# Performance work log

Measured on AMD Instinct MI355X. Metric: run time of the kernel, lower is better.

## Reference

```python
import jax, jax.numpy as jnp
import numpy as np

DIM = 1024
INTER = 2048
N_EXPERTS = 8
TOP_K = 2
ROUTE_SCALE = 1.0


def setup_inputs() -> dict:
    key = jax.random.key(0)
    ks = jax.random.split(key, 4)
    x = jax.random.normal(ks[0], (4, 2048, DIM), dtype=jnp.float32)
    # Gate weight matches nn.Parameter(torch.randn(n_experts, dim))
    Wg = jax.random.normal(ks[1], (N_EXPERTS, DIM), dtype=jnp.float32)
    W1 = jax.random.normal(ks[2], (N_EXPERTS, DIM, INTER), dtype=jnp.float32) * (1.0 / np.sqrt(DIM))
    b1 = jnp.zeros((N_EXPERTS, INTER), dtype=jnp.float32)
    W2 = jax.random.normal(ks[3], (N_EXPERTS, INTER, DIM), dtype=jnp.float32) * (1.0 / np.sqrt(INTER))
    b2 = jnp.zeros((N_EXPERTS, DIM), dtype=jnp.float32)
    return {"x": x, "Wg": Wg, "W1": W1, "b1": b1, "W2": W2, "b2": b2}


def reference(x, Wg, W1, b1, W2, b2):
    # Flatten tokens: [T, D]
    xt = x.reshape(-1, DIM)
    T = xt.shape[0]

    # --- Gate: sigmoid scores, top-k, normalized weights ---
    scores = jax.nn.sigmoid(xt @ Wg.T)                       # [T, E]
    top_w, top_idx = jax.lax.top_k(scores, TOP_K)            # [T, K]
    top_w = top_w / jnp.sum(top_w, axis=-1, keepdims=True)
    top_w = top_w * ROUTE_SCALE

    # Sparse combine weights [T, E] (top_k indices are distinct per token)
    cw = jnp.zeros((T, N_EXPERTS), dtype=xt.dtype)
    cw = cw.at[jnp.arange(T)[:, None], top_idx].set(top_w)

    # --- Experts: dense per-expert MLP, weighted combine ---
    # (dropout is identity in eval mode)
    h = jax.nn.relu(jnp.einsum('td,edh->eth', xt, W1) + b1[:, None, :])   # [E, T, H]
    eo = jnp.einsum('eth,ehd->etd', h, W2) + b2[:, None, :]               # [E, T, D]
    y = jnp.einsum('etd,te->td', eo, cw)                                  # [T, D]
    return y
```

## Files before the change

### kernel.cpp

```cpp
#include <hip/hip_runtime.h>
#include <stdint.h>

#define DIM   1024
#define INTER 2048
#define NEXP  8
#define TIMAX 136

typedef _Float16 f16;
typedef __attribute__((ext_vector_type(2))) _Float16 f16x2;
typedef __attribute__((ext_vector_type(4))) _Float16 f16x4;
typedef __attribute__((ext_vector_type(8))) _Float16 f16x8;
typedef __attribute__((ext_vector_type(4))) float    f32x4;

static __device__ __forceinline__ void gload16(const void* gsrc, void* lds) {
    __builtin_amdgcn_global_load_lds(
        (const __attribute__((address_space(1))) uint32_t*)gsrc,
        (__attribute__((address_space(3))) uint32_t*)lds,
        16, 0, 0);
}

__device__ __forceinline__ void transpose_tile(const float* __restrict__ W, f16* __restrict__ Wt,
                                               int K, int N, int e, int kb, int nb, int t,
                                               f16 (*tile)[66]) {
    const float* We  = W  + (size_t)e * K * N;
    f16*         Wte = Wt + (size_t)e * K * N;
    const int kl = t >> 4;
    const int nq = t & 15;
    #pragma unroll
    for (int pass = 0; pass < 4; ++pass) {
        int k = pass * 16 + kl;
        float4 v = *(const float4*)&We[(size_t)(kb + k) * N + nb + nq * 4];
        f16x2 lo = { (f16)v.x, (f16)v.y };
        f16x2 hi = { (f16)v.z, (f16)v.w };
        *(f16x2*)&tile[k][nq * 4]     = lo;
        *(f16x2*)&tile[k][nq * 4 + 2] = hi;
    }
    __syncthreads();
    const int n  = t >> 2;
    const int kq = t & 3;
    f16x8 o0, o1;
    #pragma unroll
    for (int i = 0; i < 8; ++i) o0[i] = tile[kq * 16 + i][n];
    #pragma unroll
    for (int i = 0; i < 8; ++i) o1[i] = tile[kq * 16 + 8 + i][n];
    f16* dst = &Wte[(size_t)(nb + n) * K + kb + kq * 16];
    *(f16x8*)dst       = o0;
    *(f16x8*)(dst + 8) = o1;
}

__global__ void preprocess_kernel(const float* __restrict__ x, const float* __restrict__ Wg,
                                  const float* __restrict__ W1, const float* __restrict__ W2,
                                  f16* __restrict__ xh, f16* __restrict__ w1t, f16* __restrict__ w2t,
                                  float* __restrict__ gw, int* __restrict__ gidx, int T) {
    __shared__ f16 tile[64][66];
    const int bid     = blockIdx.x;
    const int NB_GATE = T / 4;
    const int NB_TR1  = (INTER / 64) * (DIM / 64) * NEXP;

    if (bid < NB_GATE) {
        const int tid  = threadIdx.x;
        const int tok  = bid * 4 + (tid >> 6);
        const int lane = tid & 63;
        const float4* xr  = (const float4*)(x + (size_t)tok * DIM);
        f16*          xhr = xh + (size_t)tok * DIM;
        float s[NEXP];
        #pragma unroll
        for (int e = 0; e < NEXP; ++e) s[e] = 0.f;
        #pragma unroll
        for (int it = 0; it < 4; ++it) {
            int i = it * 64 + lane;
            float4 xv = xr[i];
            f16x4 hv = { (f16)xv.x, (f16)xv.y, (f16)xv.z, (f16)xv.w };
            *(f16x4*)(xhr + i * 4) = hv;
            #pragma unroll
            for (int e = 0; e < NEXP; ++e) {
                float4 wv = ((const float4*)(Wg + e * DIM))[i];
                s[e] += xv.x * wv.x + xv.y * wv.y + xv.z * wv.z + xv.w * wv.w;
            }
        }
        #pragma unroll
        for (int e = 0; e < NEXP; ++e) {
            #pragma unroll
            for (int off = 32; off > 0; off >>= 1) s[e] += __shfl_xor(s[e], off);
        }
        if (lane == 0) {
            float sc[NEXP];
            #pragma unroll
            for (int e = 0; e < NEXP; ++e) sc[e] = 1.f / (1.f + expf(-s[e]));
            int i0 = 0;
            #pragma unroll
            for (int e = 1; e < NEXP; ++e) if (sc[e] > sc[i0]) i0 = e;
            int i1 = -1;
            #pragma unroll
            for (int e = 0; e < NEXP; ++e) if (e != i0 && (i1 < 0 || sc[e] > sc[i1])) i1 = e;
            float w0 = sc[i0], w1 = sc[i1];
            float inv = 1.f / (w0 + w1);
            gw[2 * tok + 0] = w0 * inv;
            gw[2 * tok + 1] = w1 * inv;
            gidx[2 * tok + 0] = i0;
            gidx[2 * tok + 1] = i1;
        }
    } else if (bid < NB_GATE + NB_TR1) {
        const int b  = bid - NB_GATE;
        const int nx = b % (INTER / 64);
        const int ky = (b / (INTER / 64)) % (DIM / 64);
        const int e  = b / ((INTER / 64) * (DIM / 64));
        transpose_tile(W1, w1t, DIM, INTER, e, ky * 64, nx * 64, threadIdx.x, tile);
    } else {
        const int b  = bid - NB_GATE - NB_TR1;
        const int nx = b % (DIM / 64);
        const int ky = (b / (DIM / 64)) % (INTER / 64);
        const int e  = b / ((DIM / 64) * (INTER / 64));
        transpose_tile(W2, w2t, INTER, DIM, e, ky * 64, nx * 64, threadIdx.x, tile);
    }
}

__global__ __launch_bounds__(1024)
void route_kernel(const int* __restrict__ gidx, int* __restrict__ offsets,
                  int* __restrict__ tor, int* __restrict__ ros,
                  int* __restrict__ tileE, int* __restrict__ tileR0, int T) {
    const int tid  = threadIdx.x;
    const int lane = tid & 63;
    const int wv   = tid >> 6;
    const int NE   = 2 * T;
    __shared__ int wc[16][NEXP];
    __shared__ int rb[NEXP];

    int c[NEXP];
    #pragma unroll
    for (int e = 0; e < NEXP; ++e) c[e] = 0;
    for (int i = tid; i < NE; i += 1024) {
        int g = gidx[i];
        #pragma unroll
        for (int e = 0; e < NEXP; ++e) c[e] += (g == e) ? 1 : 0;
    }
    #pragma unroll
    for (int e = 0; e < NEXP; ++e) {
        #pragma unroll
        for (int off = 32; off > 0; off >>= 1) c[e] += __shfl_xor(c[e], off);
    }
    if (lane == 0) {
        #pragma unroll
        for (int e = 0; e < NEXP; ++e) wc[wv][e] = c[e];
    }
    __syncthreads();
    if (tid == 0) {
        int acc = 0;
        for (int e = 0; e < NEXP; ++e) {
            int t = 0;
            for (int w2 = 0; w2 < 16; ++w2) t += wc[w2][e];
            offsets[e] = acc;
            rb[e] = acc;
            acc += t;
        }
        offsets[NEXP] = acc;
        int nt = 0;
        for (int e = 0; e < NEXP; ++e)
            for (int r0 = offsets[e]; r0 < offsets[e + 1]; r0 += 128) {
                tileE[nt]  = e;
                tileR0[nt] = r0;
                ++nt;
            }
        for (; nt < TIMAX; ++nt) { tileE[nt] = -1; tileR0[nt] = 0; }
    }
    __syncthreads();

    for (int base = 0; base < NE; base += 1024) {
        int i = base + tid;
        int g = gidx[i];
        int myrank = 0;
        #pragma unroll
        for (int e = 0; e < NEXP; ++e) {
            unsigned long long m = __ballot(g == e);
            if (g == e) myrank = __popcll(m & ((1ull << lane) - 1ull));
            if (lane == 0) wc[wv][e] = __popcll(m);
        }
        __syncthreads();
        int pre = 0;
        for (int w2 = 0; w2 < wv; ++w2) pre += wc[w2][g];
        int pos = rb[g] + pre + myrank;
        tor[pos] = i >> 1;
        ros[i]   = pos;
        __syncthreads();
        if (tid < NEXP) {
            int t = 0;
            for (int w2 = 0; w2 < 16; ++w2) t += wc[w2][tid];
            rb[tid] += t;
        }
        __syncthreads();
    }
}

template<int KD, int ND, bool RELU, bool GATHER>
__global__ __launch_bounds__(256)
void moe_gemm_kernel(const f16* __restrict__ Abase, const f16* __restrict__ Bt,
                     const float* __restrict__ bias, const int* __restrict__ offsets,
                     const int* __restrict__ tok, const int* __restrict__ tileE,
                     const int* __restrict__ tileR0, f16* __restrict__ Cout) {
    constexpr int NT  = ND / 128;
    constexpr int NT2 = NT / 2;
    const int bid = blockIdx.x;
    const int xcd = bid & 7;
    const int j   = bid >> 3;
    const int nt  = (j % NT2) * 2 + (xcd & 1);
    const int tih = j / NT2;
    const int ti  = tih * 4 + (xcd >> 1);

    const int e = tileE[ti];
    if (e < 0) return;
    const int row0   = tileR0[ti];
    const int rowEnd = offsets[e + 1];
    const int n0   = nt * 128;
    const int tid  = threadIdx.x;
    const int lane = tid & 63;
    const int wid  = tid >> 6;
    const int wr   = (wid >> 1) * 64;
    const int wc   = (wid & 1) * 64;

    __shared__ __align__(16) f16 As[128 * 64];
    __shared__ __align__(16) f16 Bs[128 * 64];

    const f16* Bte = Bt + (size_t)e * ND * KD;

    int aOff[4], bOff[4], ldsOff[4];
    #pragma unroll
    for (int i = 0; i < 4; ++i) {
        int c  = i * 256 + tid;
        int r  = c >> 3;
        int kc = (c & 7) ^ (r & 7);
        ldsOff[i] = c * 8;
        int gr = row0 + r;
        if (gr >= rowEnd) gr = rowEnd - 1;
        int ar = GATHER ? tok[gr] : gr;
        aOff[i] = ar * KD + kc * 8;
        bOff[i] = (n0 + r) * KD + kc * 8;
    }

    f32x4 acc[4][4] = {};

    const int rb    = lane & 15;
    const int jbase = lane >> 4;

    constexpr int nK = KD / 64;
    for (int kt = 0; kt < nK; ++kt) {
        const int k0 = kt * 64;
        #pragma unroll
        for (int i = 0; i < 4; ++i)
            gload16(Abase + (size_t)(aOff[i] + k0), &As[ldsOff[i]]);
        #pragma unroll
        for (int i = 0; i < 4; ++i)
            gload16(Bte + (size_t)(bOff[i] + k0), &Bs[ldsOff[i]]);
        __syncthreads();

        #pragma unroll
        for (int ks = 0; ks < 2; ++ks) {
            const int sl = (((ks * 4 + jbase) ^ (rb & 7))) * 8;
            f16x8 af[4], bfr[4];
            #pragma unroll
            for (int m = 0; m < 4; ++m)
                af[m] = *(const f16x8*)&As[(wr + m * 16 + rb) * 64 + sl];
            #pragma unroll
            for (int n = 0; n < 4; ++n)
                bfr[n] = *(const f16x8*)&Bs[(wc + n * 16 + rb) * 64 + sl];
            #pragma unroll
            for (int m = 0; m < 4; ++m)
                #pragma unroll
                for (int n = 0; n < 4; ++n)
                    acc[m][n] = __builtin_amdgcn_mfma_f32_16x16x32_f16(af[m], bfr[n], acc[m][n], 0, 0, 0);
        }

        __syncthreads();
    }

    const int rowsValid = rowEnd - row0;
    #pragma unroll
    for (int m = 0; m < 4; ++m) {
        #pragma unroll
        for (int n = 0; n < 4; ++n) {
            #pragma unroll
            for (int j2 = 0; j2 < 4; ++j2) {
                int rl  = wr + m * 16 + ((lane >> 4) << 2) + j2;
                int col = n0 + wc + n * 16 + (lane & 15);
                if (rl < rowsValid) {
                    float v = acc[m][n][j2] + bias[e * ND + col];
                    if (RELU) v = fmaxf(v, 0.f);
                    Cout[(size_t)(row0 + rl) * ND + col] = (f16)v;
                }
            }
        }
    }
}

__global__ void combine_kernel(const f16* __restrict__ eo, const int* __restrict__ ros,
                               const float* __restrict__ gw, float* __restrict__ y, int T) {
    int gid = blockIdx.x * 256 + threadIdx.x;
    int t   = gid >> 7;
    if (t >= T) return;
    int c0 = (gid & 127) * 8;
    int r0 = ros[2 * t], r1 = ros[2 * t + 1];
    float w0 = gw[2 * t], w1 = gw[2 * t + 1];
    f16x8 v0 = *(const f16x8*)(eo + (size_t)r0 * DIM + c0);
    f16x8 v1 = *(const f16x8*)(eo + (size_t)r1 * DIM + c0);
    f32x4 o0, o1;
    #pragma unroll
    for (int j = 0; j < 4; ++j) o0[j] = w0 * (float)v0[j] + w1 * (float)v1[j];
    #pragma unroll
    for (int j = 0; j < 4; ++j) o1[j] = w0 * (float)v0[4 + j] + w1 * (float)v1[4 + j];
    *(f32x4*)(y + (size_t)t * DIM + c0)     = o0;
    *(f32x4*)(y + (size_t)t * DIM + c0 + 4) = o1;
}

extern "C" void kernel_launch(void* const* d_in, const int* in_sizes, int n_in,
                              void* d_out, int out_size, void* d_ws, size_t ws_size,
                              hipStream_t stream) {
    const float* x  = (const float*)d_in[0];
    const float* Wg = (const float*)d_in[1];
    const float* W1 = (const float*)d_in[2];
    const float* b1 = (const float*)d_in[3];
    const float* W2 = (const float*)d_in[4];
    const float* b2 = (const float*)d_in[5];
    float* y = (float*)d_out;
    const int T = in_sizes[0] / DIM;

    char* ws = (char*)d_ws;
    size_t off = 0;
    auto alloc = [&](size_t bytes) -> char* {
        char* p = ws + off;
        off += (bytes + 255) & ~(size_t)255;
        return p;
    };
    f16* xh   = (f16*)alloc((size_t)T * DIM * 2);
    f16* w1t  = (f16*)alloc((size_t)NEXP * DIM * INTER * 2);
    f16* w2t  = (f16*)alloc((size_t)NEXP * DIM * INTER * 2);
    f16* h    = (f16*)alloc((size_t)2 * T * INTER * 2);
    f16* eo   = (f16*)alloc((size_t)2 * T * DIM * 2);
    float* gw = (float*)alloc((size_t)T * 2 * 4);
    int* gidx = (int*)alloc((size_t)T * 2 * 4);
    int* ros  = (int*)alloc((size_t)T * 2 * 4);
    int* tor  = (int*)alloc((size_t)2 * T * 4);
    int* offsets = (int*)alloc(64 * 4);
    int* tileE   = (int*)alloc(TIMAX * 4);
    int* tileR0  = (int*)alloc(TIMAX * 4);

    const int NB_GATE = T / 4;
    const int NB_TR1  = (INTER / 64) * (DIM / 64) * NEXP;
    const int NB_TR2  = (DIM / 64) * (INTER / 64) * NEXP;
    preprocess_kernel<<<NB_GATE + NB_TR1 + NB_TR2, 256, 0, stream>>>(
        x, Wg, W1, W2, xh, w1t, w2t, gw, gidx, T);
    route_kernel<<<1, 1024, 0, stream>>>(gidx, offsets, tor, ros, tileE, tileR0, T);
    moe_gemm_kernel<DIM, INTER, true, true>
        <<<dim3((TIMAX / 4) * ((INTER / 128) / 2) * 8), 256, 0, stream>>>(
            xh, w1t, b1, offsets, tor, tileE, tileR0, h);
    moe_gemm_kernel<INTER, DIM, false, false>
        <<<dim3((TIMAX / 4) * ((DIM / 128) / 2) * 8), 256, 0, stream>>>(
            h, w2t, b2, offsets, tor, tileE, tileR0, eo);
    combine_kernel<<<(T * DIM / 8 + 255) / 256, 256, 0, stream>>>(eo, ros, gw, y, T);
}
```

Before: 319.5 us.

## Use 256x256 MoE GEMM tiles with double-buffered LDS and ping-pong MFMA scheduling

Grows each MoE GEMM workgroup from a 128x128 to a 256x256 output tile with 512 threads (8 waves, each owning 128x64), and sizes the routing tiles in 256-row chunks. LDS is double-buffered, and the loop splits each K step into four quadrant phases. Global-to-LDS loads for the next stages are issued between barriers while MFMAs run at raised priority. The aim is more data reuse per byte loaded and hiding load latency behind compute. The cost is more padding waste for partially filled expert tiles, fewer workgroups in flight (64KB LDS each), and many extra barriers.

```diff
diff --git a/kernel.cpp b/kernel.cpp
--- a/kernel.cpp
+++ b/kernel.cpp
@@ -4,7 +4,7 @@
 #define DIM   1024
 #define INTER 2048
 #define NEXP  8
-#define TIMAX 136
+#define TIMAX 72
 
 typedef _Float16 f16;
 typedef __attribute__((ext_vector_type(2))) _Float16 f16x2;
@@ -156,7 +156,7 @@
         offsets[NEXP] = acc;
         int nt = 0;
         for (int e = 0; e < NEXP; ++e)
-            for (int r0 = offsets[e]; r0 < offsets[e + 1]; r0 += 128) {
+            for (int r0 = offsets[e]; r0 < offsets[e + 1]; r0 += 256) {
                 tileE[nt]  = e;
                 tileR0[nt] = r0;
                 ++nt;
@@ -192,95 +192,150 @@
 }
 
 template<int KD, int ND, bool RELU, bool GATHER>
-__global__ __launch_bounds__(256)
+__global__ __launch_bounds__(512)
 void moe_gemm_kernel(const f16* __restrict__ Abase, const f16* __restrict__ Bt,
                      const float* __restrict__ bias, const int* __restrict__ offsets,
                      const int* __restrict__ tok, const int* __restrict__ tileE,
                      const int* __restrict__ tileR0, f16* __restrict__ Cout) {
-    constexpr int NT  = ND / 128;
+    constexpr int NT  = ND / 256;
     constexpr int NT2 = NT / 2;
     const int bid = blockIdx.x;
     const int xcd = bid & 7;
     const int j   = bid >> 3;
     const int nt  = (j % NT2) * 2 + (xcd & 1);
-    const int tih = j / NT2;
-    const int ti  = tih * 4 + (xcd >> 1);
+    const int ti  = (j / NT2) * 4 + (xcd >> 1);
 
     const int e = tileE[ti];
     if (e < 0) return;
     const int row0   = tileR0[ti];
     const int rowEnd = offsets[e + 1];
-    const int n0   = nt * 128;
+    const int n0   = nt * 256;
     const int tid  = threadIdx.x;
     const int lane = tid & 63;
     const int wid  = tid >> 6;
-    const int wr   = (wid >> 1) * 64;
-    const int wc   = (wid & 1) * 64;
-
-    __shared__ __align__(16) f16 As[128 * 64];
-    __shared__ __align__(16) f16 Bs[128 * 64];
+    const int wm   = wid >> 2;
+    const int wn   = wid & 3;
+
+    __shared__ __align__(16) f16 As[2][2][128 * 64];
+    __shared__ __align__(16) f16 Bs[2][2][128 * 64];
 
     const f16* Bte = Bt + (size_t)e * ND * KD;
 
-    int aOff[4], bOff[4], ldsOff[4];
-    #pragma unroll
-    for (int i = 0; i < 4; ++i) {
-        int c  = i * 256 + tid;
+    int aOff[2][2], bOff[2][2], ldsc[2];
+    #pragma unroll
+    for (int i = 0; i < 2; ++i) {
+        int c  = i * 512 + tid;
         int r  = c >> 3;
         int kc = (c & 7) ^ (r & 7);
-        ldsOff[i] = c * 8;
-        int gr = row0 + r;
-        if (gr >= rowEnd) gr = rowEnd - 1;
-        int ar = GATHER ? tok[gr] : gr;
-        aOff[i] = ar * KD + kc * 8;
-        bOff[i] = (n0 + r) * KD + kc * 8;
-    }
-
-    f32x4 acc[4][4] = {};
-
-    const int rb    = lane & 15;
-    const int jbase = lane >> 4;
-
-    constexpr int nK = KD / 64;
-    for (int kt = 0; kt < nK; ++kt) {
-        const int k0 = kt * 64;
-        #pragma unroll
-        for (int i = 0; i < 4; ++i)
-            gload16(Abase + (size_t)(aOff[i] + k0), &As[ldsOff[i]]);
-        #pragma unroll
-        for (int i = 0; i < 4; ++i)
-            gload16(Bte + (size_t)(bOff[i] + k0), &Bs[ldsOff[i]]);
-        __syncthreads();
-
-        #pragma unroll
-        for (int ks = 0; ks < 2; ++ks) {
-            const int sl = (((ks * 4 + jbase) ^ (rb & 7))) * 8;
-            f16x8 af[4], bfr[4];
-            #pragma unroll
-            for (int m = 0; m < 4; ++m)
-                af[m] = *(const f16x8*)&As[(wr + m * 16 + rb) * 64 + sl];
-            #pragma unroll
-            for (int n = 0; n < 4; ++n)
-                bfr[n] = *(const f16x8*)&Bs[(wc + n * 16 + rb) * 64 + sl];
+        ldsc[i] = c * 8;
+        #pragma unroll
+        for (int h = 0; h < 2; ++h) {
+            int gr = row0 + h * 128 + r;
+            if (gr >= rowEnd) gr = rowEnd - 1;
+            int ar = GATHER ? tok[gr] : gr;
+            aOff[h][i] = ar * KD + kc * 8;
+            bOff[h][i] = (n0 + h * 128 + r) * KD + kc * 8;
+        }
+    }
+
+    auto stageA = [&](int d, int kt, int h) {
+        #pragma unroll
+        for (int i = 0; i < 2; ++i)
+            gload16(Abase + (size_t)(aOff[h][i] + kt * 64), &As[d][h][ldsc[i]]);
+    };
+    auto stageB = [&](int d, int kt, int h) {
+        #pragma unroll
+        for (int i = 0; i < 2; ++i)
+            gload16(Bte + (size_t)(bOff[h][i] + kt * 64), &Bs[d][h][ldsc[i]]);
+    };
+
+    f32x4 acc[8][4] = {};
+    f16x8 af[4][2], bfA[2][2], bfB[2][2];
+
+    const int rb  = lane & 15;
+    const int sl0 = ((lane >> 4) ^ (lane & 7)) * 8;
+
+    auto readA = [&](int d, int mq) {
+        const f16* base = &As[d][wm][0];
+        #pragma unroll
+        for (int m = 0; m < 4; ++m) {
+            int ro = (mq * 64 + m * 16 + rb) * 64;
+            af[m][0] = *(const f16x8*)&base[ro + sl0];
+            af[m][1] = *(const f16x8*)&base[ro + (sl0 ^ 32)];
+        }
+    };
+    auto readB = [&](int d, int nq, f16x8 (&bf)[2][2]) {
+        const f16* base = &Bs[d][wn >> 1][0];
+        #pragma unroll
+        for (int n = 0; n < 2; ++n) {
+            int ro = ((wn & 1) * 64 + (nq * 2 + n) * 16 + rb) * 64;
+            bf[n][0] = *(const f16x8*)&base[ro + sl0];
+            bf[n][1] = *(const f16x8*)&base[ro + (sl0 ^ 32)];
+        }
+    };
+    auto domfma = [&](int mq, int nq, f16x8 (&bf)[2][2]) {
+        #pragma unroll
+        for (int ks = 0; ks < 2; ++ks)
             #pragma unroll
             for (int m = 0; m < 4; ++m)
                 #pragma unroll
-                for (int n = 0; n < 4; ++n)
-                    acc[m][n] = __builtin_amdgcn_mfma_f32_16x16x32_f16(af[m], bfr[n], acc[m][n], 0, 0, 0);
-        }
-
-        __syncthreads();
+                for (int n = 0; n < 2; ++n)
+                    acc[mq * 4 + m][nq * 2 + n] = __builtin_amdgcn_mfma_f32_16x16x32_f16(
+                        af[m][ks], bf[n][ks], acc[mq * 4 + m][nq * 2 + n], 0, 0, 0);
+    };
+
+    constexpr int nK = KD / 64;
+
+    stageA(0, 0, 0); stageA(0, 0, 1);
+    stageB(0, 0, 0); stageB(0, 0, 1);
+    stageB(1, 1, 0); stageB(1, 1, 1);
+    asm volatile("s_waitcnt vmcnt(4)" ::: "memory");
+    __builtin_amdgcn_s_barrier();
+
+    for (int t = 0; t < nK; ++t) {
+        const int d = t & 1;
+        readA(d, 0); readB(d, 0, bfA);
+        if (t + 1 < nK) stageA(d ^ 1, t + 1, 0);
+        __builtin_amdgcn_s_barrier();
+        __builtin_amdgcn_s_setprio(1);
+        domfma(0, 0, bfA);
+        __builtin_amdgcn_s_setprio(0);
+        __builtin_amdgcn_s_barrier();
+        readB(d, 1, bfB);
+        if (t + 1 < nK) stageA(d ^ 1, t + 1, 1);
+        __builtin_amdgcn_s_barrier();
+        __builtin_amdgcn_s_setprio(1);
+        domfma(0, 1, bfB);
+        __builtin_amdgcn_s_setprio(0);
+        __builtin_amdgcn_s_barrier();
+        readA(d, 1);
+        if (t + 2 < nK) stageB(d, t + 2, 0);
+        __builtin_amdgcn_s_barrier();
+        __builtin_amdgcn_s_setprio(1);
+        domfma(1, 1, bfB);
+        __builtin_amdgcn_s_setprio(0);
+        __builtin_amdgcn_s_barrier();
+        if (t + 2 < nK) stageB(d, t + 2, 1);
+        __builtin_amdgcn_s_barrier();
+        __builtin_amdgcn_s_setprio(1);
+        domfma(1, 0, bfA);
+        __builtin_amdgcn_s_setprio(0);
+        if (t + 2 < nK)      { asm volatile("s_waitcnt vmcnt(4)" ::: "memory"); }
+        else if (t + 1 < nK) { asm volatile("s_waitcnt vmcnt(0)" ::: "memory"); }
+        __builtin_amdgcn_s_barrier();
     }
 
     const int rowsValid = rowEnd - row0;
-    #pragma unroll
-    for (int m = 0; m < 4; ++m) {
+    const int wr  = wm * 128;
+    const int wcn = wn * 64;
+    #pragma unroll
+    for (int m = 0; m < 8; ++m) {
         #pragma unroll
         for (int n = 0; n < 4; ++n) {
             #pragma unroll
             for (int j2 = 0; j2 < 4; ++j2) {
                 int rl  = wr + m * 16 + ((lane >> 4) << 2) + j2;
-                int col = n0 + wc + n * 16 + (lane & 15);
+                int col = n0 + wcn + n * 16 + (lane & 15);
                 if (rl < rowsValid) {
                     float v = acc[m][n][j2] + bias[e * ND + col];
                     if (RELU) v = fmaxf(v, 0.f);
@@ -349,10 +404,10 @@
         x, Wg, W1, W2, xh, w1t, w2t, gw, gidx, T);
     route_kernel<<<1, 1024, 0, stream>>>(gidx, offsets, tor, ros, tileE, tileR0, T);
     moe_gemm_kernel<DIM, INTER, true, true>
-        <<<dim3((TIMAX / 4) * ((INTER / 128) / 2) * 8), 256, 0, stream>>>(
+        <<<dim3((TIMAX / 4) * ((INTER / 256) / 2) * 8), 512, 0, stream>>>(
             xh, w1t, b1, offsets, tor, tileE, tileR0, h);
     moe_gemm_kernel<INTER, DIM, false, false>
-        <<<dim3((TIMAX / 4) * ((DIM / 128) / 2) * 8), 256, 0, stream>>>(
+        <<<dim3((TIMAX / 4) * ((DIM / 256) / 2) * 8), 512, 0, stream>>>(
             h, w2t, b2, offsets, tor, tileE, tileR0, eo);
     combine_kernel<<<(T * DIM / 8 + 255) / 256, 256, 0, stream>>>(eo, ros, gw, y, T);
 }
```

Result: slower. 397.7 us (+24.5%).
